# Performance work log

Measured on AMD Instinct MI355X. Metric: run time of the kernel, lower is better.

## Reference

```python
import jax, jax.numpy as jnp
import numpy as np
import math

NUM_HEADS = 16
HEAD_DIM = 64
NUM_BUCKETS = 256
MAX_DISTANCE = 16384
ROPE_BASE = 10000.0


def _rel_pos_bucket(rel):
    # faithful to RelativePositionEncoding._relative_position_bucket
    ab = jnp.abs(rel)
    max_exact = NUM_BUCKETS // 4  # 64
    half = NUM_BUCKETS // 2       # 128
    is_small = ab < max_exact
    safe = jnp.maximum(ab, 1).astype(jnp.float32)
    large = max_exact + (jnp.log(safe / max_exact) / math.log(MAX_DISTANCE / max_exact) * (half - max_exact)).astype(jnp.int32)
    large = jnp.minimum(large, half - 1)
    bucket = jnp.where(is_small, ab, large)
    bucket = jnp.where(rel < 0, half + bucket, bucket)
    return bucket


def _rope_cos_sin(seq_len):
    # RotaryPositionEncoding with rope dim = 2*head_dim: num_features = head_dim,
    # inv_freq over arange(0, head_dim, 2)/head_dim, interleaved repeat to head_dim
    inv_freq = 1.0 / (ROPE_BASE ** (jnp.arange(0, HEAD_DIM, 2, dtype=jnp.float32) / HEAD_DIM))
    pos = jnp.arange(seq_len, dtype=jnp.float32)
    freqs = pos[:, None] * inv_freq[None, :]          # [S, HEAD_DIM//2]
    cos = jnp.repeat(jnp.cos(freqs), 2, axis=-1)      # [S, HEAD_DIM]
    sin = jnp.repeat(jnp.sin(freqs), 2, axis=-1)
    return cos, sin


def _rotate_half(t):
    h = t.shape[-1] // 2
    return jnp.concatenate([-t[..., h:], t[..., :h]], axis=-1)


def setup_inputs() -> dict:
    key = jax.random.key(0)
    ks = jax.random.split(key, 6)
    B, S, E = 2, 2048, 1024
    x = jax.random.normal(ks[0], (B, S, E), dtype=jnp.float32)
    Wq = jax.random.normal(ks[1], (E, E), dtype=jnp.float32) * 0.02
    Wk = jax.random.normal(ks[2], (E, E), dtype=jnp.float32) * 0.02
    Wv = jax.random.normal(ks[3], (E, E), dtype=jnp.float32) * 0.02
    Wo = jax.random.normal(ks[4], (E, E), dtype=jnp.float32) * 0.02
    rel_emb = jax.random.normal(ks[5], (NUM_BUCKETS, NUM_HEADS, HEAD_DIM), dtype=jnp.float32) * 0.02
    return {"x": x, "Wq": Wq, "Wk": Wk, "Wv": Wv, "Wo": Wo, "rel_emb": rel_emb}


def reference(x, Wq, Wk, Wv, Wo, rel_emb):
    B, S, E = x.shape
    H, D = NUM_HEADS, HEAD_DIM

    def split_heads(t):
        return t.reshape(B, S, H, D).transpose(0, 2, 1, 3)  # [B,H,S,D]

    q = split_heads(x @ Wq)
    k = split_heads(x @ Wk)
    v = split_heads(x @ Wv)

    # inline RoPE on q/k (cos/sin broadcast over batch & heads)
    cos, sin = _rope_cos_sin(S)  # [S, D]
    q = q * cos + _rotate_half(q) * sin
    k = k * cos + _rotate_half(k) * sin

    # relative-position bucket bias: q . rel_emb[bucket(i-j)]
    pos = jnp.arange(S)
    bucket = _rel_pos_bucket(pos[:, None] - pos[None, :])      # [S, S]
    q_rel = jnp.einsum('bhqd,nhd->bhqn', q, rel_emb)           # [B,H,S,NUM_BUCKETS]
    bias = jnp.take_along_axis(q_rel, bucket[None, None, :, :], axis=-1)  # [B,H,S,S]

    scale = 1.0 / math.sqrt(D)
    scores = (jnp.einsum('bhqd,bhkd->bhqk', q, k) + bias) * scale

    causal = pos[:, None] >= pos[None, :]
    scores = jnp.where(causal[None, None], scores, jnp.float32(-1e9))
    attn = jax.nn.softmax(scores, axis=-1)

    out = jnp.einsum('bhqk,bhkd->bhqd', attn, v)
    out = out.transpose(0, 2, 1, 3).reshape(B, S, E)
    return out @ Wo
```

## Files before the change

### kernel.cpp

```cpp
#include <hip/hip_runtime.h>
#include <hip/hip_bf16.h>
#include <math.h>


typedef __attribute__((ext_vector_type(8))) short bf16x8;
typedef __attribute__((ext_vector_type(4))) float f32x4;

static __device__ __forceinline__ unsigned short f2bf(float x) {
    unsigned u = __float_as_uint(x);
    unsigned r = (u + 0x7fffu + ((u >> 16) & 1u)) >> 16;
    return (unsigned short)r;
}
static __device__ __forceinline__ float bf2f(unsigned short h) {
    return __uint_as_float(((unsigned)h) << 16);
}
static __device__ __forceinline__ unsigned cvtpk(float lo, float hi) {
    unsigned r;
    asm("v_cvt_pk_bf16_f32 %0, %1, %2" : "=v"(r) : "v"(lo), "v"(hi));
    return r;
}
static __device__ __forceinline__ float fexp2(float x) {
    return __builtin_amdgcn_exp2f(x);
}

#define GLOAD16(gp, lp)                                                            \
    __builtin_amdgcn_global_load_lds(                                              \
        (const __attribute__((address_space(1))) unsigned int*)(gp),               \
        (__attribute__((address_space(3))) unsigned int*)(lp), 16, 0, 0)

__global__ void prep(const float* __restrict__ x,
                     const float* __restrict__ W0, const float* __restrict__ W1,
                     const float* __restrict__ W2, const float* __restrict__ W3,
                     const float* __restrict__ rel,
                     unsigned short* __restrict__ xb,
                     unsigned short* __restrict__ T0, unsigned short* __restrict__ T1,
                     unsigned short* __restrict__ T2, unsigned short* __restrict__ T3,
                     unsigned short* __restrict__ relTb)
{
    __shared__ unsigned short tls[64][65];
    const int id  = blockIdx.x;
    const int tid = threadIdx.x;
    if (id < 2048) {
        const size_t t = (size_t)id * 256 + tid;
        const float4* p = (const float4*)(x + t*8);
        float4 a = p[0], b = p[1];
        unsigned w0 = cvtpk(a.x, a.y), w1 = cvtpk(a.z, a.w);
        unsigned w2 = cvtpk(b.x, b.y), w3 = cvtpk(b.z, b.w);
        *(uint4*)(xb + t*8) = make_uint4(w0, w1, w2, w3);
    } else if (id < 3072) {
        const int local = id - 2048;
        const int z  = local >> 8;
        const float* W = (z == 0) ? W0 : (z == 1) ? W1 : (z == 2) ? W2 : W3;
        unsigned short* Wt = (z == 0) ? T0 : (z == 1) ? T1 : (z == 2) ? T2 : T3;
        const int bb  = local & 255;
        const int bxt = bb & 15;
        const int byt = bb >> 4;
        const int r   = tid >> 2;
        const int c0  = (tid & 3) * 16;
        const float* src = W + (size_t)(byt*64 + r)*1024 + bxt*64 + c0;
#pragma unroll
        for (int j = 0; j < 4; ++j) {
            float4 vv = ((const float4*)src)[j];
            tls[c0 + j*4 + 0][r] = f2bf(vv.x);
            tls[c0 + j*4 + 1][r] = f2bf(vv.y);
            tls[c0 + j*4 + 2][r] = f2bf(vv.z);
            tls[c0 + j*4 + 3][r] = f2bf(vv.w);
        }
        __syncthreads();
        unsigned short* dst = Wt + (size_t)(bxt*64 + r)*1024 + byt*64 + c0;
        unsigned w[8];
#pragma unroll
        for (int j = 0; j < 8; ++j)
            w[j] = (unsigned)tls[r][c0 + 2*j] | ((unsigned)tls[r][c0 + 2*j + 1] << 16);
        *(uint4*)(dst)     = make_uint4(w[0], w[1], w[2], w[3]);
        *(uint4*)(dst + 8) = make_uint4(w[4], w[5], w[6], w[7]);
    } else {
        const int t  = (id - 3072) * 256 + tid;
        const int d0 = (t & 7) * 8;
        const int n  = (t >> 3) & 127;
        const int h  = t >> 10;
        const float* src = rel + ((size_t)(n*16 + h))*64 + d0;
        float4 a = ((const float4*)src)[0], b = ((const float4*)src)[1];
        unsigned w0 = cvtpk(a.x, a.y), w1 = cvtpk(a.z, a.w);
        unsigned w2 = cvtpk(b.x, b.y), w3 = cvtpk(b.z, b.w);
        *(uint4*)(relTb + (size_t)h*8192 + n*64 + d0) = make_uint4(w0, w1, w2, w3);
    }
}

#define GEMM_STAGE(t, buf)                                                             \
    {                                                                                  \
        const int k0s = (t) * 64;                                                      \
        _Pragma("unroll")                                                              \
        for (int j = 0; j < 4; ++j) {                                                  \
            GLOAD16(agp + (size_t)(j*32 + srow)*1024 + k0s, &Als[buf][0] + j*2048 + tid*8); \
            GLOAD16(bgp + (size_t)(j*32 + srow)*1024 + k0s, &Bls[buf][0] + j*2048 + tid*8); \
        }                                                                              \
    }

#define GEMM_COMPUTE(buf)                                                              \
    {                                                                                  \
        _Pragma("unroll")                                                              \
        for (int ks = 0; ks < 2; ++ks) {                                               \
            bf16x8 af[4], bfr[4];                                                      \
            _Pragma("unroll")                                                          \
            for (int m = 0; m < 4; ++m)                                                \
                af[m] = *(const bf16x8*)&Als[buf][(wr + m*16 + (lane & 15))*64 + ks*32 + (lane >> 4)*8]; \
            _Pragma("unroll")                                                          \
            for (int n = 0; n < 4; ++n)                                                \
                bfr[n] = *(const bf16x8*)&Bls[buf][(wc + n*16 + (lane & 15))*64 + ks*32 + (lane >> 4)*8]; \
            _Pragma("unroll")                                                          \
            for (int m = 0; m < 4; ++m)                                                \
                _Pragma("unroll")                                                      \
                for (int n = 0; n < 4; ++n)                                            \
                    acc[m][n] = __builtin_amdgcn_mfma_f32_16x16x32_bf16(af[m], bfr[n], acc[m][n], 0, 0, 0); \
        }                                                                              \
    }

__global__ __launch_bounds__(256) void gemm_qkv(const unsigned short* __restrict__ A,
    const unsigned short* __restrict__ wtq, const unsigned short* __restrict__ wtk,
    const unsigned short* __restrict__ wtv,
    float* __restrict__ qf, float* __restrict__ kf, unsigned short* __restrict__ vTb)
{
    __shared__ __align__(16) unsigned short Als[2][8192];
    __shared__ __align__(16) unsigned short Bls[2][8192];
    const int z = blockIdx.z;
    const unsigned short* Bt = (z == 0) ? wtq : (z == 1) ? wtk : wtv;

    const int tid  = threadIdx.x;
    const int wave = tid >> 6, lane = tid & 63;
    const int wr = (wave >> 1) * 64, wc = (wave & 1) * 64;
    const int bx = blockIdx.x, by = blockIdx.y;
    const int srow = tid >> 3;
    const unsigned short* agp = A  + (size_t)(by*128)*1024 + (tid & 7)*8;
    const unsigned short* bgp = Bt + (size_t)(bx*128)*1024 + (tid & 7)*8;

    f32x4 acc[4][4];
#pragma unroll
    for (int m = 0; m < 4; ++m)
#pragma unroll
        for (int n = 0; n < 4; ++n) acc[m][n] = (f32x4)0.f;

    GEMM_STAGE(0, 0);
    __syncthreads();
    int cur = 0;
    for (int t = 0; t < 16; ++t) {
        if (t < 15) GEMM_STAGE(t + 1, cur ^ 1);
        GEMM_COMPUTE(cur);
        __syncthreads();
        cur ^= 1;
    }

#pragma unroll
    for (int m = 0; m < 4; ++m) {
        const int r0 = by*128 + wr + m*16 + (lane >> 4)*4;
#pragma unroll
        for (int n = 0; n < 4; ++n) {
            const int col = bx*128 + wc + n*16 + (lane & 15);
            if (z == 2) {
                const int bb = r0 >> 11, ss = r0 & 2047;
                const int hh = col >> 6, dd = col & 63;
                unsigned r01 = cvtpk(acc[m][n][0], acc[m][n][1]);
                unsigned r23 = cvtpk(acc[m][n][2], acc[m][n][3]);
                *(uint2*)(vTb + (((size_t)bb*16 + hh)*64 + dd)*2048 + ss) = make_uint2(r01, r23);
            } else {
                float* C = z ? kf : qf;
#pragma unroll
                for (int rg = 0; rg < 4; ++rg) {
                    const int row = r0 + rg;
                    const int bb = row >> 11, ss = row & 2047;
                    const int hh = col >> 6,  dd = col & 63;
                    C[(((size_t)bb*16 + hh)*2048 + ss)*64 + dd] = acc[m][n][rg];
                }
            }
        }
    }
}

__global__ __launch_bounds__(256) void gemm_o(const unsigned short* __restrict__ A,
                                              const unsigned short* __restrict__ Bt,
                                              float* __restrict__ C)
{
    __shared__ __align__(16) unsigned short Als[2][8192];
    __shared__ __align__(16) unsigned short Bls[2][8192];
    const int tid  = threadIdx.x;
    const int wave = tid >> 6, lane = tid & 63;
    const int wr = (wave >> 1) * 64, wc = (wave & 1) * 64;
    const int bx = blockIdx.x, by = blockIdx.y;
    const int srow = tid >> 3;
    const unsigned short* agp = A  + (size_t)(by*128)*1024 + (tid & 7)*8;
    const unsigned short* bgp = Bt + (size_t)(bx*128)*1024 + (tid & 7)*8;

    f32x4 acc[4][4];
#pragma unroll
    for (int m = 0; m < 4; ++m)
#pragma unroll
        for (int n = 0; n < 4; ++n) acc[m][n] = (f32x4)0.f;

    GEMM_STAGE(0, 0);
    __syncthreads();
    int cur = 0;
    for (int t = 0; t < 16; ++t) {
        if (t < 15) GEMM_STAGE(t + 1, cur ^ 1);
        GEMM_COMPUTE(cur);
        __syncthreads();
        cur ^= 1;
    }

#pragma unroll
    for (int m = 0; m < 4; ++m) {
        const int r0 = by*128 + wr + m*16 + (lane >> 4)*4;
#pragma unroll
        for (int n = 0; n < 4; ++n) {
            const int col = bx*128 + wc + n*16 + (lane & 15);
#pragma unroll
            for (int rg = 0; rg < 4; ++rg)
                C[(size_t)(r0 + rg)*1024 + col] = acc[m][n][rg];
        }
    }
}

__global__ void rope_bf16(const float* __restrict__ qf, const float* __restrict__ kf,
                          unsigned short* __restrict__ qb, unsigned short* __restrict__ kb)
{
    const int t = blockIdx.x * 256 + threadIdx.x;
    const int ten = t >> 21;
    const int r = t & ((1 << 21) - 1);
    const int dd = r & 31;
    const int s  = (r >> 5) & 2047;
    const int bh = r >> 16;
    const float* p = ten ? kf : qf;
    unsigned short* o = ten ? kb : qb;
    const size_t base = ((size_t)bh*2048 + s)*64;
    const float x0 = p[base + dd];
    const float x1 = p[base + dd + 32];
    const float f0 = (float)(dd >> 1);
    const float CC = 0.41524101186092029f;
    const float if0 = exp2f(-f0 * CC);
    const float if1 = exp2f(-(f0 + 16.f) * CC);
    const float a0 = (float)s * if0;
    const float a1 = (float)s * if1;
    o[base + dd]      = f2bf(x0 * cosf(a0) - x1 * sinf(a0));
    o[base + dd + 32] = f2bf(x1 * cosf(a1) + x0 * sinf(a1));
}

__global__ __launch_bounds__(256) void qrel_mfma(const unsigned short* __restrict__ qb,
                                                 const unsigned short* __restrict__ relTb,
                                                 unsigned short* __restrict__ qrelb)
{
    __shared__ __align__(16) unsigned short Rls[8192];
    __shared__ __align__(16) unsigned short Qls[8192];
    const int tid  = threadIdx.x;
    const int wave = tid >> 6, lane = tid & 63;
    const int wr = (wave >> 1) * 64;
    const int wc = (wave & 1) * 64;
    const int s0 = blockIdx.x * 128;
    const int bh = blockIdx.y;
    const int h  = bh & 15;

    const unsigned short* qsrc = qb + ((size_t)bh*2048 + s0)*64;
    const unsigned short* rsrc = relTb + (size_t)h*8192;
#pragma unroll
    for (int j = 0; j < 4; ++j) {
        GLOAD16(rsrc + j*2048 + tid*8, &Rls[0] + j*2048 + tid*8);
        GLOAD16(qsrc + j*2048 + tid*8, &Qls[0] + j*2048 + tid*8);
    }

    f32x4 acc[4][4];
#pragma unroll
    for (int m = 0; m < 4; ++m)
#pragma unroll
        for (int n = 0; n < 4; ++n) acc[m][n] = (f32x4)0.f;

    __syncthreads();

#pragma unroll
    for (int ks = 0; ks < 2; ++ks) {
        bf16x8 rf[4], qf[4];
#pragma unroll
        for (int m = 0; m < 4; ++m)
            rf[m] = *(const bf16x8*)&Rls[(wr + m*16 + (lane & 15))*64 + ks*32 + (lane >> 4)*8];
#pragma unroll
        for (int n = 0; n < 4; ++n)
            qf[n] = *(const bf16x8*)&Qls[(wc + n*16 + (lane & 15))*64 + ks*32 + (lane >> 4)*8];
#pragma unroll
        for (int m = 0; m < 4; ++m)
#pragma unroll
            for (int n = 0; n < 4; ++n)
                acc[m][n] = __builtin_amdgcn_mfma_f32_16x16x32_bf16(rf[m], qf[n], acc[m][n], 0, 0, 0);
    }

#pragma unroll
    for (int m = 0; m < 4; ++m) {
        const int bkt0 = wr + m*16 + (lane >> 4)*4;
#pragma unroll
        for (int n = 0; n < 4; ++n) {
            const int srow = s0 + wc + n*16 + (lane & 15);
            unsigned r01 = cvtpk(acc[m][n][0], acc[m][n][1]);
            unsigned r23 = cvtpk(acc[m][n][2], acc[m][n][3]);
            *(uint2*)(qrelb + ((size_t)bh*2048 + srow)*128 + bkt0) = make_uint2(r01, r23);
        }
    }
}

__global__ __launch_bounds__(256) void flash_mfma(
    const unsigned short* __restrict__ qb, const unsigned short* __restrict__ kb,
    const unsigned short* __restrict__ vT, const unsigned short* __restrict__ qrelb,
    unsigned short* __restrict__ ctxb)
{
    __shared__ __align__(16) unsigned short kls[4096];
    __shared__ __align__(16) unsigned short vtls[4096];
    __shared__ __align__(16) unsigned short qrels[64*136];

    const int tid = threadIdx.x;
    const int id  = blockIdx.x;
    const int bh  = id & 31;
    const int px  = id >> 5;

    const int w   = tid >> 6;
    const int l   = tid & 63;
    const int q15 = l & 15;
    const int g   = l >> 4;

    const size_t headoff = (size_t)bh * 2048 * 64;
    const unsigned short* gbase;
    int jstride;
    char* lbase;
    if (tid < 128) { gbase = kb + headoff; jstride = 64; lbase = (char*)kls; }
    else           { gbase = vT + headoff; jstride = 1;  lbase = (char*)vtls; }
    int soff[4]; char* ldst[4];
#pragma unroll
    for (int i = 0; i < 4; ++i) {
        const int D = (tid & 127)*16 + i*2048;
        const int r = D >> 7, c = (D >> 4) & 7;
        soff[i] = (tid < 128) ? (r*64 + ((c ^ (r & 7))*8))
                              : (r*2048 + ((c ^ (r & 7))*8));
        ldst[i] = lbase + D;
    }

    const float SCL = 0.1803368801111204f;
    const int qrow_lds = (w*16 + q15) * 136;
    const int srcA = ((2*g) & 3)*16 + q15;
    const int srcB = ((2*g + 1) & 3)*16 + q15;

    for (int pp = 0; pp < 2; ++pp) {
        const int bxc = pp ? (31 - px) : px;
        const int i0  = bxc * 64;
        const int iq  = i0 + w*16 + q15;

        __syncthreads();
        for (int idx = tid; idx < 1024; idx += 256) {
            const int r = idx >> 4, c8 = idx & 15;
            uint4 vv = *(const uint4*)(qrelb + ((size_t)bh*2048 + i0 + r)*128 + c8*8);
            *(uint4*)&qrels[r*136 + c8*8] = vv;
        }

        bf16x8 qf0, qf1;
        {
            const unsigned short* qrow = qb + ((size_t)bh*2048 + i0 + w*16 + q15)*64;
            qf0 = *(const bf16x8*)(qrow + g*8);
            qf1 = *(const bf16x8*)(qrow + 32 + g*8);
        }

        f32x4 acc[4];
#pragma unroll
        for (int d = 0; d < 4; ++d) acc[d] = (f32x4)0.f;
        float mrun = -INFINITY, lsum = 0.f;

        const int ntiles = bxc + 1;
        for (int t = 0; t < ntiles; ++t) {
            const int j0 = t * 64;
            __syncthreads();
            {
                const unsigned short* gt = gbase + (size_t)j0 * jstride;
#pragma unroll
                for (int i = 0; i < 4; ++i) GLOAD16(gt + soff[i], ldst[i]);
            }
            __syncthreads();

            f32x4 s[4];
#pragma unroll
            for (int ss = 0; ss < 4; ++ss) s[ss] = (f32x4)0.f;
#pragma unroll
            for (int ks = 0; ks < 2; ++ks) {
                const bf16x8 qq = ks ? qf1 : qf0;
                const int gr = ((ks*4 + g) ^ (q15 & 7)) * 8;
#pragma unroll
                for (int ss = 0; ss < 4; ++ss) {
                    bf16x8 kf = *(const bf16x8*)&kls[(ss*16 + q15)*64 + gr];
                    s[ss] = __builtin_amdgcn_mfma_f32_16x16x32_bf16(kf, qq, s[ss], 0, 0, 0);
                }
            }
            float sv[16];
            float tmax = -INFINITY;
#pragma unroll
            for (int ss = 0; ss < 4; ++ss) {
#pragma unroll
                for (int r = 0; r < 4; ++r) {
                    const int rel = iq - (j0 + ss*16 + g*4 + r);
                    const int bi = rel < 0 ? 0 : rel;
                    int bkt;
                    if (bi < 64) bkt = bi;
                    else {
                        bkt = 64 + (int)(__log2f((float)bi) * 8.0f - 48.0f);
                        bkt = bkt > 127 ? 127 : bkt;
                    }
                    const float bias = bf2f(qrels[qrow_lds + bkt]);
                    const float val = (s[ss][r] + bias) * SCL;
                    sv[ss*4 + r] = (rel >= 0) ? val : -1e30f;
                    tmax = fmaxf(tmax, sv[ss*4 + r]);
                }
            }
            tmax = fmaxf(tmax, __shfl_xor(tmax, 16));
            tmax = fmaxf(tmax, __shfl_xor(tmax, 32));

            float newm = mrun;
            if (!__all(tmax - mrun <= 8.0f)) {
                newm = fmaxf(mrun, tmax);
                const float corr = fexp2(mrun - newm);
                lsum *= corr;
#pragma unroll
                for (int d = 0; d < 4; ++d) {
                    acc[d][0] *= corr; acc[d][1] *= corr; acc[d][2] *= corr; acc[d][3] *= corr;
                }
                mrun = newm;
            }

            float p[16], ps = 0.f;
#pragma unroll
            for (int j = 0; j < 16; ++j) { p[j] = fexp2(sv[j] - newm); ps += p[j]; }
            ps += __shfl_xor(ps, 16);
            ps += __shfl_xor(ps, 32);
            lsum += ps;

#pragma unroll
            for (int ck = 0; ck < 2; ++ck) {
                unsigned w00 = cvtpk(p[8*ck+0], p[8*ck+1]);
                unsigned w01 = cvtpk(p[8*ck+2], p[8*ck+3]);
                unsigned w10 = cvtpk(p[8*ck+4], p[8*ck+5]);
                unsigned w11 = cvtpk(p[8*ck+6], p[8*ck+7]);
                unsigned a0 = (unsigned)__shfl((int)w00, srcA);
                unsigned b0 = (unsigned)__shfl((int)w10, srcA);
                unsigned a1 = (unsigned)__shfl((int)w01, srcA);
                unsigned b1 = (unsigned)__shfl((int)w11, srcA);
                unsigned a2 = (unsigned)__shfl((int)w00, srcB);
                unsigned b2 = (unsigned)__shfl((int)w10, srcB);
                unsigned a3 = (unsigned)__shfl((int)w01, srcB);
                unsigned b3 = (unsigned)__shfl((int)w11, srcB);
                union { unsigned u[4]; bf16x8 v; } pu;
                pu.u[0] = (g < 2) ? a0 : b0;
                pu.u[1] = (g < 2) ? a1 : b1;
                pu.u[2] = (g < 2) ? a2 : b2;
                pu.u[3] = (g < 2) ? a3 : b3;
#pragma unroll
                for (int dblk = 0; dblk < 4; ++dblk) {
                    const int d2 = dblk*16 + q15;
                    bf16x8 vf = *(const bf16x8*)&vtls[d2*64 + (((ck*4 + g) ^ (d2 & 7))*8)];
                    acc[dblk] = __builtin_amdgcn_mfma_f32_16x16x32_bf16(vf, pu.v, acc[dblk], 0, 0, 0);
                }
            }
        }

        const float inv = 1.0f / lsum;
        const int s2 = i0 + w*16 + q15;
        const int b2 = bh >> 4, hh = bh & 15;
        unsigned short* obase = ctxb + (((size_t)b2*2048 + s2)*16 + hh)*64;
#pragma unroll
        for (int dblk = 0; dblk < 4; ++dblk) {
            const int d0 = dblk*16 + g*4;
            unsigned r01 = cvtpk(acc[dblk][0]*inv, acc[dblk][1]*inv);
            unsigned r23 = cvtpk(acc[dblk][2]*inv, acc[dblk][3]*inv);
            *(uint2*)(obase + d0) = make_uint2(r01, r23);
        }
    }
}

extern "C" void kernel_launch(void* const* d_in, const int* in_sizes, int n_in,
                              void* d_out, int out_size, void* d_ws, size_t ws_size,
                              hipStream_t stream)
{
    const float* x   = (const float*)d_in[0];
    const float* Wq  = (const float*)d_in[1];
    const float* Wk  = (const float*)d_in[2];
    const float* Wv  = (const float*)d_in[3];
    const float* Wo  = (const float*)d_in[4];
    const float* rel = (const float*)d_in[5];

    float* ws = (float*)d_ws;
    float* qf32 = ws;
    float* kf32 = ws + 4194304;
    unsigned short* qb    = (unsigned short*)(ws + 8388608);
    unsigned short* kbb   = (unsigned short*)(ws + 10485760);
    unsigned short* qrelb = (unsigned short*)(ws + 12582912);
    unsigned short* vTb   = (unsigned short*)(ws + 16777216);
    unsigned short* xb    = (unsigned short*)(ws + 18874368);
    unsigned short* wtq   = (unsigned short*)(ws + 20971520);
    unsigned short* wtk   = (unsigned short*)(ws + 21495808);
    unsigned short* wtv   = (unsigned short*)(ws + 22020096);
    unsigned short* wto   = (unsigned short*)(ws + 22544384);
    unsigned short* relTb = (unsigned short*)(ws + 23068672);
    unsigned short* ctxb  = (unsigned short*)ws;

    prep<<<3136, 256, 0, stream>>>(x, Wq, Wk, Wv, Wo, rel, xb, wtq, wtk, wtv, wto, relTb);
    gemm_qkv<<<dim3(8, 32, 3), 256, 0, stream>>>(xb, wtq, wtk, wtv, qf32, kf32, vTb);
    rope_bf16<<<16384, 256, 0, stream>>>(qf32, kf32, qb, kbb);
    qrel_mfma<<<dim3(16, 32), 256, 0, stream>>>(qb, relTb, qrelb);
    flash_mfma<<<512, 256, 0, stream>>>(qb, kbb, vTb, qrelb, ctxb);
    gemm_o<<<dim3(8, 32), 256, 0, stream>>>(ctxb, wto, (float*)d_out);
}
```

Measured before the change: 205.0 us.

## Fuse RoPE into QKV GEMM epilogue and double-buffer K/V tiles in flash kernel

```diff
diff --git a/kernel.cpp b/kernel.cpp
--- a/kernel.cpp
+++ b/kernel.cpp
@@ -119,7 +119,8 @@
 __global__ __launch_bounds__(256) void gemm_qkv(const unsigned short* __restrict__ A,
     const unsigned short* __restrict__ wtq, const unsigned short* __restrict__ wtk,
     const unsigned short* __restrict__ wtv,
-    float* __restrict__ qf, float* __restrict__ kf, unsigned short* __restrict__ vTb)
+    unsigned short* __restrict__ qb, unsigned short* __restrict__ kbb,
+    unsigned short* __restrict__ vTb)
 {
     __shared__ __align__(16) unsigned short Als[2][8192];
     __shared__ __align__(16) unsigned short Bls[2][8192];
@@ -150,26 +151,46 @@
         cur ^= 1;
     }
 
-#pragma unroll
-    for (int m = 0; m < 4; ++m) {
-        const int r0 = by*128 + wr + m*16 + (lane >> 4)*4;
-#pragma unroll
-        for (int n = 0; n < 4; ++n) {
-            const int col = bx*128 + wc + n*16 + (lane & 15);
-            if (z == 2) {
+    if (z == 2) {
+#pragma unroll
+        for (int m = 0; m < 4; ++m) {
+            const int r0 = by*128 + wr + m*16 + (lane >> 4)*4;
+#pragma unroll
+            for (int n = 0; n < 4; ++n) {
+                const int col = bx*128 + wc + n*16 + (lane & 15);
                 const int bb = r0 >> 11, ss = r0 & 2047;
                 const int hh = col >> 6, dd = col & 63;
                 unsigned r01 = cvtpk(acc[m][n][0], acc[m][n][1]);
                 unsigned r23 = cvtpk(acc[m][n][2], acc[m][n][3]);
                 *(uint2*)(vTb + (((size_t)bb*16 + hh)*64 + dd)*2048 + ss) = make_uint2(r01, r23);
-            } else {
-                float* C = z ? kf : qf;
+            }
+        }
+    } else {
+        unsigned short* O = z ? kbb : qb;
+        const float CC = 0.41524101186092029f;
+#pragma unroll
+        for (int n = 0; n < 2; ++n) {
+            const int dd = n*16 + (lane & 15);
+            const float if0 = exp2f(-(float)(dd >> 1) * CC);
+            const float if1 = exp2f(-(float)(16 + (dd >> 1)) * CC);
+            const int col = bx*128 + wc + n*16 + (lane & 15);
+            const int hh = col >> 6;
+#pragma unroll
+            for (int m = 0; m < 4; ++m) {
+                const int r0 = by*128 + wr + m*16 + (lane >> 4)*4;
 #pragma unroll
                 for (int rg = 0; rg < 4; ++rg) {
                     const int row = r0 + rg;
-                    const int bb = row >> 11, ss = row & 2047;
-                    const int hh = col >> 6,  dd = col & 63;
-                    C[(((size_t)bb*16 + hh)*2048 + ss)*64 + dd] = acc[m][n][rg];
+                    const int bb = row >> 11, s = row & 2047;
+                    const float x0 = acc[m][n][rg];
+                    const float x1 = acc[m][n + 2][rg];
+                    const float a0 = (float)s * if0;
+                    const float a1 = (float)s * if1;
+                    const float o0 = x0 * __cosf(a0) - x1 * __sinf(a0);
+                    const float o1 = x1 * __cosf(a1) + x0 * __sinf(a1);
+                    unsigned short* ob = O + (((size_t)bb*16 + hh)*2048 + s)*64 + dd;
+                    ob[0]  = f2bf(o0);
+                    ob[32] = f2bf(o1);
                 }
             }
         }
@@ -219,30 +240,6 @@
     }
 }
 
-__global__ void rope_bf16(const float* __restrict__ qf, const float* __restrict__ kf,
-                          unsigned short* __restrict__ qb, unsigned short* __restrict__ kb)
-{
-    const int t = blockIdx.x * 256 + threadIdx.x;
-    const int ten = t >> 21;
-    const int r = t & ((1 << 21) - 1);
-    const int dd = r & 31;
-    const int s  = (r >> 5) & 2047;
-    const int bh = r >> 16;
-    const float* p = ten ? kf : qf;
-    unsigned short* o = ten ? kb : qb;
-    const size_t base = ((size_t)bh*2048 + s)*64;
-    const float x0 = p[base + dd];
-    const float x1 = p[base + dd + 32];
-    const float f0 = (float)(dd >> 1);
-    const float CC = 0.41524101186092029f;
-    const float if0 = exp2f(-f0 * CC);
-    const float if1 = exp2f(-(f0 + 16.f) * CC);
-    const float a0 = (float)s * if0;
-    const float a1 = (float)s * if1;
-    o[base + dd]      = f2bf(x0 * cosf(a0) - x1 * sinf(a0));
-    o[base + dd + 32] = f2bf(x1 * cosf(a1) + x0 * sinf(a1));
-}
-
 __global__ __launch_bounds__(256) void qrel_mfma(const unsigned short* __restrict__ qb,
                                                  const unsigned short* __restrict__ relTb,
                                                  unsigned short* __restrict__ qrelb)
@@ -307,8 +304,8 @@
     const unsigned short* __restrict__ vT, const unsigned short* __restrict__ qrelb,
     unsigned short* __restrict__ ctxb)
 {
-    __shared__ __align__(16) unsigned short kls[4096];
-    __shared__ __align__(16) unsigned short vtls[4096];
+    __shared__ __align__(16) unsigned short kls[2][4096];
+    __shared__ __align__(16) unsigned short vtls[2][4096];
     __shared__ __align__(16) unsigned short qrels[64*136];
 
     const int tid = threadIdx.x;
@@ -324,17 +321,16 @@
     const size_t headoff = (size_t)bh * 2048 * 64;
     const unsigned short* gbase;
     int jstride;
-    char* lbase;
-    if (tid < 128) { gbase = kb + headoff; jstride = 64; lbase = (char*)kls; }
-    else           { gbase = vT + headoff; jstride = 1;  lbase = (char*)vtls; }
-    int soff[4]; char* ldst[4];
+    if (tid < 128) { gbase = kb + headoff; jstride = 64; }
+    else           { gbase = vT + headoff; jstride = 1;  }
+    int soff[4], doff[4];
 #pragma unroll
     for (int i = 0; i < 4; ++i) {
         const int D = (tid & 127)*16 + i*2048;
         const int r = D >> 7, c = (D >> 4) & 7;
         soff[i] = (tid < 128) ? (r*64 + ((c ^ (r & 7))*8))
                               : (r*2048 + ((c ^ (r & 7))*8));
-        ldst[i] = lbase + D;
+        doff[i] = D;
     }
 
     const float SCL = 0.1803368801111204f;
@@ -342,6 +338,7 @@
     const int srcA = ((2*g) & 3)*16 + q15;
     const int srcB = ((2*g + 1) & 3)*16 + q15;
 
+    int cur = 0;
     for (int pp = 0; pp < 2; ++pp) {
         const int bxc = pp ? (31 - px) : px;
         const int i0  = bxc * 64;
@@ -353,6 +350,11 @@
             uint4 vv = *(const uint4*)(qrelb + ((size_t)bh*2048 + i0 + r)*128 + c8*8);
             *(uint4*)&qrels[r*136 + c8*8] = vv;
         }
+        {
+            char* lb = (tid < 128) ? (char*)kls[cur] : (char*)vtls[cur];
+#pragma unroll
+            for (int i = 0; i < 4; ++i) GLOAD16(gbase + soff[i], lb + doff[i]);
+        }
 
         bf16x8 qf0, qf1;
         {
@@ -366,16 +368,17 @@
         for (int d = 0; d < 4; ++d) acc[d] = (f32x4)0.f;
         float mrun = -INFINITY, lsum = 0.f;
 
+        __syncthreads();
+
         const int ntiles = bxc + 1;
         for (int t = 0; t < ntiles; ++t) {
             const int j0 = t * 64;
-            __syncthreads();
-            {
-                const unsigned short* gt = gbase + (size_t)j0 * jstride;
-#pragma unroll
-                for (int i = 0; i < 4; ++i) GLOAD16(gt + soff[i], ldst[i]);
-            }
-            __syncthreads();
+            if (t + 1 < ntiles) {
+                const unsigned short* gt = gbase + (size_t)(j0 + 64) * jstride;
+                char* lb = (tid < 128) ? (char*)kls[cur ^ 1] : (char*)vtls[cur ^ 1];
+#pragma unroll
+                for (int i = 0; i < 4; ++i) GLOAD16(gt + soff[i], lb + doff[i]);
+            }
 
             f32x4 s[4];
 #pragma unroll
@@ -386,7 +389,7 @@
                 const int gr = ((ks*4 + g) ^ (q15 & 7)) * 8;
 #pragma unroll
                 for (int ss = 0; ss < 4; ++ss) {
-                    bf16x8 kf = *(const bf16x8*)&kls[(ss*16 + q15)*64 + gr];
+                    bf16x8 kf = *(const bf16x8*)&kls[cur][(ss*16 + q15)*64 + gr];
                     s[ss] = __builtin_amdgcn_mfma_f32_16x16x32_bf16(kf, qq, s[ss], 0, 0, 0);
                 }
             }
@@ -454,10 +457,13 @@
 #pragma unroll
                 for (int dblk = 0; dblk < 4; ++dblk) {
                     const int d2 = dblk*16 + q15;
-                    bf16x8 vf = *(const bf16x8*)&vtls[d2*64 + (((ck*4 + g) ^ (d2 & 7))*8)];
+                    bf16x8 vf = *(const bf16x8*)&vtls[cur][d2*64 + (((ck*4 + g) ^ (d2 & 7))*8)];
                     acc[dblk] = __builtin_amdgcn_mfma_f32_16x16x32_bf16(vf, pu.v, acc[dblk], 0, 0, 0);
                 }
             }
+
+            __syncthreads();
+            cur ^= 1;
         }
 
         const float inv = 1.0f / lsum;
@@ -486,8 +492,6 @@
     const float* rel = (const float*)d_in[5];
 
     float* ws = (float*)d_ws;
-    float* qf32 = ws;
-    float* kf32 = ws + 4194304;
     unsigned short* qb    = (unsigned short*)(ws + 8388608);
     unsigned short* kbb   = (unsigned short*)(ws + 10485760);
     unsigned short* qrelb = (unsigned short*)(ws + 12582912);
@@ -501,8 +505,7 @@
     unsigned short* ctxb  = (unsigned short*)ws;
 
     prep<<<3136, 256, 0, stream>>>(x, Wq, Wk, Wv, Wo, rel, xb, wtq, wtk, wtv, wto, relTb);
-    gemm_qkv<<<dim3(8, 32, 3), 256, 0, stream>>>(xb, wtq, wtk, wtv, qf32, kf32, vTb);
-    rope_bf16<<<16384, 256, 0, stream>>>(qf32, kf32, qb, kbb);
+    gemm_qkv<<<dim3(8, 32, 3), 256, 0, stream>>>(xb, wtq, wtk, wtv, qb, kbb, vTb);
     qrel_mfma<<<dim3(16, 32), 256, 0, stream>>>(qb, relTb, qrelb);
     flash_mfma<<<512, 256, 0, stream>>>(qb, kbb, vTb, qrelb, ctxb);
     gemm_o<<<dim3(8, 32), 256, 0, stream>>>(ctxb, wto, (float*)d_out);
```

After: 191.0 us. -6.8%, faster.
